# Kernel tuning notes

Measured on AMD Instinct MI355X. Metric: run time of the kernel, lower is better.

## Reference

```python
import jax, jax.numpy as jnp
import numpy as np

N = 50000   # nodes
E = 800000  # edges
D = 200     # h_dim == out_dim
R = 500     # num_rels
L = 2       # num_hidden_layers
RRELU_SLOPE = (1.0 / 8.0 + 1.0 / 3.0) / 2.0  # eval-mode F.rrelu negative slope


def _rrelu(x):
    return jnp.where(x >= 0, x, x * jnp.float32(RRELU_SLOPE))


def setup_inputs() -> dict:
    key = jax.random.key(0)
    ks = jax.random.split(key, 10)
    s = np.float32(1.0 / np.sqrt(D))  # ~xavier scale
    return {
        "init_ent_emb": jax.random.normal(ks[0], (N, D), jnp.float32),
        "rel_emb": jax.random.normal(ks[1], (R, D), jnp.float32),
        "weight_neighbor": jax.random.normal(ks[2], (L, D, D), jnp.float32) * s,
        "loop_weight": jax.random.normal(ks[3], (L, D, D), jnp.float32) * s,
        "evolve_loop_weight": jax.random.normal(ks[4], (L, D, D), jnp.float32) * s,
        "norm": jax.random.uniform(ks[5], (N, 1), jnp.float32),
        "src": jax.random.randint(ks[6], (E,), 0, N, dtype=jnp.int32),
        "dst": jax.random.randint(ks[7], (E,), 0, N, dtype=jnp.int32),
        "etype": jax.random.randint(ks[8], (E,), 0, R, dtype=jnp.int32),
        "node_id": jnp.arange(N, dtype=jnp.int32),
    }


def reference(init_ent_emb, rel_emb, weight_neighbor, loop_weight,
              evolve_loop_weight, norm, src, dst, etype, node_id):
    # g.ndata['h'] = init_ent_emb[node_id]
    h = init_ent_emb[node_id]                                    # [N, D]
    # mask of nodes with in-degree > 0 (fixed across layers)
    indeg = jnp.zeros((N,), jnp.float32).at[dst].add(1.0)
    has_in = (indeg > 0)[:, None]                                # [N, 1]
    for l in range(L):
        # loop message: loop_weight where in-degree>0, evolve_loop_weight otherwise
        loop_msg = jnp.where(has_in,
                             h @ loop_weight[l],
                             h @ evolve_loop_weight[l])          # [N, D]
        # per-edge message: (h_src + rel_emb[etype]) @ W_neighbor
        msg = (h[src] + rel_emb[etype]) @ weight_neighbor[l]     # [E, D]
        # sum-scatter to destination nodes, then per-node norm (apply_func)
        agg = jax.ops.segment_sum(msg, dst, num_segments=N)      # [N, D]
        h = _rrelu(agg * norm + loop_msg)
    return h
```

## Files before the change

### kernel.cpp

```cpp
#include <hip/hip_runtime.h>

#define D 200
#define RRELU_SLOPE 0.22916666666666666f
#define STRIDE 96
#define PAD 8

typedef unsigned short u16;
typedef unsigned int u32;

using bf16x8 = __attribute__((ext_vector_type(8))) short;
using f32x4  = __attribute__((ext_vector_type(4))) float;

__device__ __forceinline__ float rrelu(float x) {
    return x >= 0.0f ? x : x * RRELU_SLOPE;
}
__device__ __forceinline__ float bf2f(u32 u) {
    union { u32 i; float f; } c; c.i = u << 16; return c.f;
}
__device__ __forceinline__ u32 f2bf(float f) {
    union { float f; u32 i; } c; c.f = f;
    return (c.i + 0x7fffu + ((c.i >> 16) & 1u)) >> 16;
}
__device__ __forceinline__ u32 pack2(float x, float y) {
    return f2bf(x) | (f2bf(y) << 16);
}
__device__ __forceinline__ void gll16(const void* g, void* l) {
    __builtin_amdgcn_global_load_lds((const __attribute__((address_space(1))) void*)g,
                                     (__attribute__((address_space(3))) void*)l,
                                     16, 0, 0);
}

__device__ __forceinline__ void accu4(uint4 q, float* acc) {
    acc[0] += bf2f(q.x & 0xffffu); acc[1] += bf2f(q.x >> 16);
    acc[2] += bf2f(q.y & 0xffffu); acc[3] += bf2f(q.y >> 16);
    acc[4] += bf2f(q.z & 0xffffu); acc[5] += bf2f(q.z >> 16);
    acc[6] += bf2f(q.w & 0xffffu); acc[7] += bf2f(q.w >> 16);
}


__global__ void prep_k(const float* __restrict__ rel, const float* __restrict__ Wn,
                       const float* __restrict__ Wl, u16* __restrict__ relb,
                       u16* __restrict__ Bt, u16* __restrict__ hb0d,
                       u16* __restrict__ hb1d, int* __restrict__ noin_cnt) {
    int i = blockIdx.x * blockDim.x + threadIdx.x;
    if (i == 0) *noin_cnt = 0;
    if (i < 200) { hb0d[i] = 0; hb1d[i] = 0; }
    if (i < 100200) relb[i] = (i < 100000) ? (u16)f2bf(rel[i]) : (u16)0;
    if (i < 2 * 256 * 416) {
        int l = i / (256 * 416);
        int rem = i % (256 * 416);
        int c = rem / 416;
        int k = rem % 416;
        float v = 0.0f;
        if (c < 200 && k < 400)
            v = (k < 200) ? Wn[(size_t)l * 40000 + k * 200 + c]
                          : Wl[(size_t)l * 40000 + (k - 200) * 200 + c];
        Bt[i] = (u16)f2bf(v);
    }
}


__global__ void scatter_k(const int* __restrict__ dst, const int* __restrict__ src,
                          const int* __restrict__ etype, int* __restrict__ cnt,
                          u32* __restrict__ ep, int E) {
    int e = blockIdx.x * blockDim.x + threadIdx.x;
    if (e < E) {
        int d = dst[e];
        int c = atomicAdd(&cnt[d], 1);
        if (c < STRIDE)
            ep[(size_t)d * STRIDE + c] = (u32)src[e] | ((u32)etype[e] << 17);
    }
}

__global__ void pad_k(const int* __restrict__ cnt, u32* __restrict__ ep, u32 dummy,
                      int* __restrict__ noin, int* __restrict__ noin_cnt, int N) {
    int v = blockIdx.x * blockDim.x + threadIdx.x;
    if (v >= N) return;
    int c = cnt[v];
    if (c == 0) noin[atomicAdd(noin_cnt, 1)] = v;
    int e = (c + PAD - 1) & ~(PAD - 1);
    for (int i = c; i < e; ++i) ep[(size_t)v * STRIDE + i] = dummy;
}


__global__ void gather_k(const float* __restrict__ init, const int* __restrict__ nid,
                         u16* __restrict__ hb, int N) {
    int lane = threadIdx.x & 63;
    int v = blockIdx.x * 4 + (threadIdx.x >> 6);
    if (v >= N || lane >= 50) return;
    float4 f = *(const float4*)(init + (size_t)nid[v] * D + lane * 4);
    uint2 o;
    o.x = pack2(f.x, f.y);
    o.y = pack2(f.z, f.w);
    *(uint2*)(hb + (size_t)v * D + lane * 4) = o;
}


__global__ void gagg0_k(const u16* __restrict__ hb, const u16* __restrict__ relb,
                        const u32* __restrict__ ep, const int* __restrict__ cnt,
                        const float* __restrict__ norm,
                        u16* __restrict__ aggb, u16* __restrict__ relsumb, int N) {
    int lane = threadIdx.x & 63;
    int wave = threadIdx.x >> 6;
    int li = lane & 31;
    int v = blockIdx.x * 8 + wave * 2 + (lane >> 5);
    if (v >= N || li >= 25) return;
    size_t lo = (size_t)li * 8;
    const u16* hbL = hb + lo;
    const u16* rbL = relb + lo;
    int c = cnt[v];
    int rv = (c + PAD - 1) >> 3;
    int beg = v * STRIDE;
    float a[8] = {}, rr[8] = {};
    for (int r = 0; r < rv; ++r) {
        int ib = beg + r * PAD;
        u32 p[8];
#pragma unroll
        for (int j = 0; j < 8; ++j) p[j] = ep[ib + j];
        uint4 qh[8], qr[8];
#pragma unroll
        for (int j = 0; j < 8; ++j)
            qh[j] = *(const uint4*)(hbL + (size_t)(p[j] & 0x1FFFF) * D);
#pragma unroll
        for (int j = 0; j < 8; ++j)
            qr[j] = *(const uint4*)(rbL + (size_t)((p[j] >> 17) & 0x3FF) * D);
#pragma unroll
        for (int j = 0; j < 8; ++j) { accu4(qh[j], a); accu4(qr[j], rr); }
    }
    uint4 rs;
    rs.x = pack2(rr[0], rr[1]); rs.y = pack2(rr[2], rr[3]);
    rs.z = pack2(rr[4], rr[5]); rs.w = pack2(rr[6], rr[7]);
    *(uint4*)(relsumb + (size_t)v * D + lo) = rs;
    float nv = norm[v];
    uint4 o;
    o.x = pack2((a[0] + rr[0]) * nv, (a[1] + rr[1]) * nv);
    o.y = pack2((a[2] + rr[2]) * nv, (a[3] + rr[3]) * nv);
    o.z = pack2((a[4] + rr[4]) * nv, (a[5] + rr[5]) * nv);
    o.w = pack2((a[6] + rr[6]) * nv, (a[7] + rr[7]) * nv);
    *(uint4*)(aggb + (size_t)v * D + lo) = o;
}


__global__ void gagg1_k(const u16* __restrict__ hb, const u32* __restrict__ ep,
                        const int* __restrict__ cnt, const float* __restrict__ norm,
                        const u16* __restrict__ addb, u16* __restrict__ outb, int N) {
    int lane = threadIdx.x & 63;
    int wave = threadIdx.x >> 6;
    int li = lane & 31;
    int v = blockIdx.x * 8 + wave * 2 + (lane >> 5);
    if (v >= N || li >= 25) return;
    size_t lo = (size_t)li * 8;
    const u16* hbL = hb + lo;
    int c = cnt[v];
    int rv = (c + PAD - 1) >> 3;
    int beg = v * STRIDE;
    float a[8] = {};
    for (int r = 0; r < rv; ++r) {
        int ib = beg + r * PAD;
        u32 p[8];
#pragma unroll
        for (int j = 0; j < 8; ++j) p[j] = ep[ib + j];
        uint4 q[8];
#pragma unroll
        for (int j = 0; j < 8; ++j)
            q[j] = *(const uint4*)(hbL + (size_t)(p[j] & 0x1FFFF) * D);
#pragma unroll
        for (int j = 0; j < 8; ++j) accu4(q[j], a);
    }
    {
        uint4 q = *(const uint4*)(addb + (size_t)v * D + lo);
        accu4(q, a);
    }
    float nv = norm[v];
    uint4 o;
    o.x = pack2(a[0] * nv, a[1] * nv);
    o.y = pack2(a[2] * nv, a[3] * nv);
    o.z = pack2(a[4] * nv, a[5] * nv);
    o.w = pack2(a[6] * nv, a[7] * nv);
    *(uint4*)(outb + (size_t)v * D + lo) = o;
}


__global__ __launch_bounds__(256) void gemm_k(
        const u16* __restrict__ Aagg, const u16* __restrict__ Ah,
        const u16* __restrict__ Bt,
        float* __restrict__ outF, u16* __restrict__ outB, int M) {
    __shared__ __align__(16) u16 As[128 * 32];
    __shared__ __align__(16) u16 Bs[64 * 32];
    int tid = threadIdx.x;
    int lane = tid & 63;
    int wave = tid >> 6;
    int rowBase = blockIdx.x * 128;
    int colBase = blockIdx.y * 64;
    int wr = (wave >> 1) * 64;
    int wc = (wave & 1) * 32;
    int m = lane & 15;
    int kq = (lane >> 4) * 8;

    int srow = tid >> 2;
    int kg = (tid & 3) * 8;

    u16* ldsA0 = As + ((size_t)(wave * 64) * 8);
    u16* ldsA1 = As + ((size_t)(256 + wave * 64) * 8);
    u16* ldsB  = Bs + ((size_t)(wave * 64) * 8);

    f32x4 acc[4][2] = {};

    for (int k0 = 0; k0 < 416; k0 += 32) {
        int k = k0 + kg;
        {
            const u16* g0 = (k < 200) ? Aagg + (size_t)(rowBase + srow) * D + k
                                      : Ah + (size_t)(rowBase + srow) * D + (k - 200);
            gll16(g0, ldsA0);
            const u16* g1 = (k < 200) ? Aagg + (size_t)(rowBase + srow + 64) * D + k
                                      : Ah + (size_t)(rowBase + srow + 64) * D + (k - 200);
            gll16(g1, ldsA1);
            const u16* gb = Bt + (size_t)(colBase + srow) * 416 + k;
            gll16(gb, ldsB);
        }
        __syncthreads();

        bf16x8 a0 = *(const bf16x8*)(As + (wr + m) * 32 + kq);
        bf16x8 a1 = *(const bf16x8*)(As + (wr + 16 + m) * 32 + kq);
        bf16x8 a2 = *(const bf16x8*)(As + (wr + 32 + m) * 32 + kq);
        bf16x8 a3 = *(const bf16x8*)(As + (wr + 48 + m) * 32 + kq);
        bf16x8 b0 = *(const bf16x8*)(Bs + (wc + m) * 32 + kq);
        bf16x8 b1 = *(const bf16x8*)(Bs + (wc + 16 + m) * 32 + kq);
        acc[0][0] = __builtin_amdgcn_mfma_f32_16x16x32_bf16(a0, b0, acc[0][0], 0, 0, 0);
        acc[0][1] = __builtin_amdgcn_mfma_f32_16x16x32_bf16(a0, b1, acc[0][1], 0, 0, 0);
        acc[1][0] = __builtin_amdgcn_mfma_f32_16x16x32_bf16(a1, b0, acc[1][0], 0, 0, 0);
        acc[1][1] = __builtin_amdgcn_mfma_f32_16x16x32_bf16(a1, b1, acc[1][1], 0, 0, 0);
        acc[2][0] = __builtin_amdgcn_mfma_f32_16x16x32_bf16(a2, b0, acc[2][0], 0, 0, 0);
        acc[2][1] = __builtin_amdgcn_mfma_f32_16x16x32_bf16(a2, b1, acc[2][1], 0, 0, 0);
        acc[3][0] = __builtin_amdgcn_mfma_f32_16x16x32_bf16(a3, b0, acc[3][0], 0, 0, 0);
        acc[3][1] = __builtin_amdgcn_mfma_f32_16x16x32_bf16(a3, b1, acc[3][1], 0, 0, 0);
        __syncthreads();
    }

    int cRow = (lane >> 4) * 4;
    int cCol = lane & 15;
#pragma unroll
    for (int i = 0; i < 4; ++i) {
#pragma unroll
        for (int j = 0; j < 2; ++j) {
            int col = colBase + wc + j * 16 + cCol;
            if (col >= 200) continue;
#pragma unroll
            for (int r = 0; r < 4; ++r) {
                int row = rowBase + wr + i * 16 + cRow + r;
                if (row < M) {
                    float val = rrelu(acc[i][j][r]);
                    if (outF) outF[(size_t)row * D + col] = val;
                    if (outB) outB[(size_t)row * D + col] = (u16)f2bf(val);
                }
            }
        }
    }
}


__global__ void fixup_k(const u16* __restrict__ hb, const float* __restrict__ We,
                        const int* __restrict__ noin, const int* __restrict__ noin_cnt,
                        float* __restrict__ outF, u16* __restrict__ outB) {
    int cnt = *noin_cnt;
    for (int i = blockIdx.x; i < cnt; i += gridDim.x) {
        int v = noin[i];
        int j = threadIdx.x;
        if (j < D) {
            float acc = 0.0f;
            for (int k = 0; k < D; ++k)
                acc += bf2f(hb[(size_t)v * D + k]) * We[(size_t)k * D + j];
            float r = rrelu(acc);
            if (outF) outF[(size_t)v * D + j] = r;
            if (outB) outB[(size_t)v * D + j] = (u16)f2bf(r);
        }
    }
}

extern "C" void kernel_launch(void* const* d_in, const int* in_sizes, int n_in,
                              void* d_out, int out_size, void* d_ws, size_t ws_size,
                              hipStream_t stream) {
    const float* init  = (const float*)d_in[0];
    const float* rel   = (const float*)d_in[1];
    const float* Wn    = (const float*)d_in[2];
    const float* Wl    = (const float*)d_in[3];
    const float* We    = (const float*)d_in[4];
    const float* norm  = (const float*)d_in[5];
    const int* src     = (const int*)d_in[6];
    const int* dst     = (const int*)d_in[7];
    const int* etype   = (const int*)d_in[8];
    const int* node_id = (const int*)d_in[9];
    float* out = (float*)d_out;

    int N = in_sizes[5];
    int E = in_sizes[6];
    size_t NP = (size_t)N + 256;

    char* w = (char*)d_ws;
    auto carve = [&](size_t bytes) {
        char* p = w;
        w += (bytes + 255) & ~(size_t)255;
        return p;
    };
    u16* hb0     = (u16*)carve(NP * D * sizeof(u16));
    u16* hb1     = (u16*)carve(NP * D * sizeof(u16));
    u16* aggb    = (u16*)carve(NP * D * sizeof(u16));
    u16* relsumb = (u16*)carve((size_t)N * D * sizeof(u16));
    u16* relb    = (u16*)carve((size_t)501 * D * sizeof(u16));
    u16* Bt      = (u16*)carve((size_t)2 * 256 * 416 * sizeof(u16));
    int* cnt     = (int*)carve((size_t)N * sizeof(int));
    u32* epack   = (u32*)carve((size_t)N * STRIDE * sizeof(u32));
    int* noin    = (int*)carve((size_t)N * sizeof(int));
    int* noin_cnt = (int*)carve(sizeof(int));

    (void)hipMemsetAsync(cnt, 0, (size_t)N * sizeof(int), stream);

    int prepN = 2 * 256 * 416;
    prep_k<<<(prepN + 255) / 256, 256, 0, stream>>>(rel, Wn, Wl, relb, Bt,
                                                    hb0 + (size_t)N * D,
                                                    hb1 + (size_t)N * D, noin_cnt);
    scatter_k<<<(E + 255) / 256, 256, 0, stream>>>(dst, src, etype, cnt, epack, E);
    u32 dummy = (u32)N | (500u << 17);
    pad_k<<<(N + 255) / 256, 256, 0, stream>>>(cnt, epack, dummy, noin, noin_cnt, N);
    gather_k<<<(N + 3) / 4, 256, 0, stream>>>(init, node_id, hb0, N);

    dim3 gg((N + 127) / 128, 4);

    gagg0_k<<<(N + 7) / 8, 256, 0, stream>>>(hb0, relb, epack, cnt, norm,
                                             aggb, relsumb, N);
    gemm_k<<<gg, 256, 0, stream>>>(aggb, hb0, Bt, nullptr, hb1, N);
    fixup_k<<<8, 256, 0, stream>>>(hb0, We, noin, noin_cnt, nullptr, hb1);

    gagg1_k<<<(N + 7) / 8, 256, 0, stream>>>(hb1, epack, cnt, norm,
                                             relsumb, aggb, N);
    gemm_k<<<gg, 256, 0, stream>>>(aggb, hb1, Bt + 256 * 416, out, nullptr, N);
    fixup_k<<<8, 256, 0, stream>>>(hb1, We + D * D, noin, noin_cnt, out, nullptr);
}
```

Baseline: 375.8 us.

## Restructure gather-aggregate kernels as persistent one-node-per-wave loops with packed accumulation

Both edge-aggregation kernels now give one whole wave per node, with 50 lanes each loading 4 bf16 values via 8-byte loads, instead of half-wave per node with 16-byte loads. The grid becomes a fixed 2048-block persistent loop over nodes. The next group of packed edge indices is prefetched while the current gathers are in flight, and accumulation uses float2 vectors so packed adds can be emitted. The edge buffer gets extra padding so the prefetch can read past the end safely. The aim is better memory-level parallelism and less launch and tail imbalance, at the cost of smaller per-lane loads and more waves per node.

```diff
diff --git a/kernel.cpp b/kernel.cpp
--- a/kernel.cpp
+++ b/kernel.cpp
@@ -10,6 +10,7 @@
 
 using bf16x8 = __attribute__((ext_vector_type(8))) short;
 using f32x4  = __attribute__((ext_vector_type(4))) float;
+using f32x2  = __attribute__((ext_vector_type(2))) float;
 
 __device__ __forceinline__ float rrelu(float x) {
     return x >= 0.0f ? x : x * RRELU_SLOPE;
@@ -30,11 +31,12 @@
                                      16, 0, 0);
 }
 
-__device__ __forceinline__ void accu4(uint4 q, float* acc) {
-    acc[0] += bf2f(q.x & 0xffffu); acc[1] += bf2f(q.x >> 16);
-    acc[2] += bf2f(q.y & 0xffffu); acc[3] += bf2f(q.y >> 16);
-    acc[4] += bf2f(q.z & 0xffffu); acc[5] += bf2f(q.z >> 16);
-    acc[6] += bf2f(q.w & 0xffffu); acc[7] += bf2f(q.w >> 16);
+__device__ __forceinline__ void accw(u32 w, f32x2& acc) {
+    union { u32 i; float f; } lo, hi;
+    lo.i = w << 16;
+    hi.i = w & 0xffff0000u;
+    f32x2 t; t[0] = lo.f; t[1] = hi.f;
+    acc += t;
 }
 
 
@@ -96,88 +98,94 @@
 }
 
 
-__global__ void gagg0_k(const u16* __restrict__ hb, const u16* __restrict__ relb,
-                        const u32* __restrict__ ep, const int* __restrict__ cnt,
-                        const float* __restrict__ norm,
-                        u16* __restrict__ aggb, u16* __restrict__ relsumb, int N) {
+__global__ __launch_bounds__(256) void gagg0_k(
+        const u16* __restrict__ hb, const u16* __restrict__ relb,
+        const u32* __restrict__ ep, const int* __restrict__ cnt,
+        const float* __restrict__ norm,
+        u16* __restrict__ aggb, u16* __restrict__ relsumb, int N, int NW) {
     int lane = threadIdx.x & 63;
-    int wave = threadIdx.x >> 6;
-    int li = lane & 31;
-    int v = blockIdx.x * 8 + wave * 2 + (lane >> 5);
-    if (v >= N || li >= 25) return;
-    size_t lo = (size_t)li * 8;
-    const u16* hbL = hb + lo;
-    const u16* rbL = relb + lo;
-    int c = cnt[v];
-    int rv = (c + PAD - 1) >> 3;
-    int beg = v * STRIDE;
-    float a[8] = {}, rr[8] = {};
-    for (int r = 0; r < rv; ++r) {
-        int ib = beg + r * PAD;
+    int wid = __builtin_amdgcn_readfirstlane(blockIdx.x * 4 + (threadIdx.x >> 6));
+    if (lane >= 50) return;
+    const u16* hbL = hb + lane * 4;
+    const u16* rbL = relb + lane * 4;
+    for (int v = wid; v < N; v += NW) {
+        int c = cnt[v];
+        if (c > STRIDE) c = STRIDE;
+        int rv = (c + PAD - 1) >> 3;
+        const u32* pp = ep + (size_t)v * STRIDE;
+        f32x2 a0 = {0.0f, 0.0f}, a1 = {0.0f, 0.0f};
+        f32x2 r0 = {0.0f, 0.0f}, r1 = {0.0f, 0.0f};
         u32 p[8];
 #pragma unroll
-        for (int j = 0; j < 8; ++j) p[j] = ep[ib + j];
-        uint4 qh[8], qr[8];
-#pragma unroll
-        for (int j = 0; j < 8; ++j)
-            qh[j] = *(const uint4*)(hbL + (size_t)(p[j] & 0x1FFFF) * D);
-#pragma unroll
-        for (int j = 0; j < 8; ++j)
-            qr[j] = *(const uint4*)(rbL + (size_t)((p[j] >> 17) & 0x3FF) * D);
-#pragma unroll
-        for (int j = 0; j < 8; ++j) { accu4(qh[j], a); accu4(qr[j], rr); }
-    }
-    uint4 rs;
-    rs.x = pack2(rr[0], rr[1]); rs.y = pack2(rr[2], rr[3]);
-    rs.z = pack2(rr[4], rr[5]); rs.w = pack2(rr[6], rr[7]);
-    *(uint4*)(relsumb + (size_t)v * D + lo) = rs;
-    float nv = norm[v];
-    uint4 o;
-    o.x = pack2((a[0] + rr[0]) * nv, (a[1] + rr[1]) * nv);
-    o.y = pack2((a[2] + rr[2]) * nv, (a[3] + rr[3]) * nv);
-    o.z = pack2((a[4] + rr[4]) * nv, (a[5] + rr[5]) * nv);
-    o.w = pack2((a[6] + rr[6]) * nv, (a[7] + rr[7]) * nv);
-    *(uint4*)(aggb + (size_t)v * D + lo) = o;
-}
-
-
-__global__ void gagg1_k(const u16* __restrict__ hb, const u32* __restrict__ ep,
-                        const int* __restrict__ cnt, const float* __restrict__ norm,
-                        const u16* __restrict__ addb, u16* __restrict__ outb, int N) {
+        for (int j = 0; j < 8; ++j) p[j] = pp[j];
+        for (int r = 0; r < rv; ++r) {
+            uint2 qh[8], qr[8];
+#pragma unroll
+            for (int j = 0; j < 8; ++j)
+                qh[j] = *(const uint2*)(hbL + (size_t)(p[j] & 0x1FFFFu) * D);
+#pragma unroll
+            for (int j = 0; j < 8; ++j)
+                qr[j] = *(const uint2*)(rbL + (size_t)((p[j] >> 17) & 0x3FFu) * D);
+#pragma unroll
+            for (int j = 0; j < 8; ++j) p[j] = pp[(size_t)(r + 1) * 8 + j];
+#pragma unroll
+            for (int j = 0; j < 8; ++j) {
+                accw(qh[j].x, a0); accw(qh[j].y, a1);
+                accw(qr[j].x, r0); accw(qr[j].y, r1);
+            }
+        }
+        uint2 rs;
+        rs.x = pack2(r0[0], r0[1]);
+        rs.y = pack2(r1[0], r1[1]);
+        *(uint2*)(relsumb + (size_t)v * D + lane * 4) = rs;
+        float nv = norm[v];
+        uint2 o;
+        o.x = pack2((a0[0] + r0[0]) * nv, (a0[1] + r0[1]) * nv);
+        o.y = pack2((a1[0] + r1[0]) * nv, (a1[1] + r1[1]) * nv);
+        *(uint2*)(aggb + (size_t)v * D + lane * 4) = o;
+    }
+}
+
+
+__global__ __launch_bounds__(256) void gagg1_k(
+        const u16* __restrict__ hb, const u32* __restrict__ ep,
+        const int* __restrict__ cnt, const float* __restrict__ norm,
+        const u16* __restrict__ addb, u16* __restrict__ outb, int N, int NW) {
     int lane = threadIdx.x & 63;
-    int wave = threadIdx.x >> 6;
-    int li = lane & 31;
-    int v = blockIdx.x * 8 + wave * 2 + (lane >> 5);
-    if (v >= N || li >= 25) return;
-    size_t lo = (size_t)li * 8;
-    const u16* hbL = hb + lo;
-    int c = cnt[v];
-    int rv = (c + PAD - 1) >> 3;
-    int beg = v * STRIDE;
-    float a[8] = {};
-    for (int r = 0; r < rv; ++r) {
-        int ib = beg + r * PAD;
+    int wid = __builtin_amdgcn_readfirstlane(blockIdx.x * 4 + (threadIdx.x >> 6));
+    if (lane >= 50) return;
+    const u16* hbL = hb + lane * 4;
+    for (int v = wid; v < N; v += NW) {
+        int c = cnt[v];
+        if (c > STRIDE) c = STRIDE;
+        int rv = (c + PAD - 1) >> 3;
+        const u32* pp = ep + (size_t)v * STRIDE;
+        f32x2 a0 = {0.0f, 0.0f}, a1 = {0.0f, 0.0f};
         u32 p[8];
 #pragma unroll
-        for (int j = 0; j < 8; ++j) p[j] = ep[ib + j];
-        uint4 q[8];
-#pragma unroll
-        for (int j = 0; j < 8; ++j)
-            q[j] = *(const uint4*)(hbL + (size_t)(p[j] & 0x1FFFF) * D);
-#pragma unroll
-        for (int j = 0; j < 8; ++j) accu4(q[j], a);
-    }
-    {
-        uint4 q = *(const uint4*)(addb + (size_t)v * D + lo);
-        accu4(q, a);
-    }
-    float nv = norm[v];
-    uint4 o;
-    o.x = pack2(a[0] * nv, a[1] * nv);
-    o.y = pack2(a[2] * nv, a[3] * nv);
-    o.z = pack2(a[4] * nv, a[5] * nv);
-    o.w = pack2(a[6] * nv, a[7] * nv);
-    *(uint4*)(outb + (size_t)v * D + lo) = o;
+        for (int j = 0; j < 8; ++j) p[j] = pp[j];
+        for (int r = 0; r < rv; ++r) {
+            uint2 q[8];
+#pragma unroll
+            for (int j = 0; j < 8; ++j)
+                q[j] = *(const uint2*)(hbL + (size_t)(p[j] & 0x1FFFFu) * D);
+#pragma unroll
+            for (int j = 0; j < 8; ++j) p[j] = pp[(size_t)(r + 1) * 8 + j];
+#pragma unroll
+            for (int j = 0; j < 8; ++j) {
+                accw(q[j].x, a0); accw(q[j].y, a1);
+            }
+        }
+        {
+            uint2 q = *(const uint2*)(addb + (size_t)v * D + lane * 4);
+            accw(q.x, a0); accw(q.y, a1);
+        }
+        float nv = norm[v];
+        uint2 o;
+        o.x = pack2(a0[0] * nv, a0[1] * nv);
+        o.y = pack2(a1[0] * nv, a1[1] * nv);
+        *(uint2*)(outb + (size_t)v * D + lane * 4) = o;
+    }
 }
 
 
@@ -309,7 +317,7 @@
     u16* relb    = (u16*)carve((size_t)501 * D * sizeof(u16));
     u16* Bt      = (u16*)carve((size_t)2 * 256 * 416 * sizeof(u16));
     int* cnt     = (int*)carve((size_t)N * sizeof(int));
-    u32* epack   = (u32*)carve((size_t)N * STRIDE * sizeof(u32));
+    u32* epack   = (u32*)carve(((size_t)N * STRIDE + PAD) * sizeof(u32));
     int* noin    = (int*)carve((size_t)N * sizeof(int));
     int* noin_cnt = (int*)carve(sizeof(int));
 
@@ -326,13 +334,16 @@
 
     dim3 gg((N + 127) / 128, 4);
 
-    gagg0_k<<<(N + 7) / 8, 256, 0, stream>>>(hb0, relb, epack, cnt, norm,
-                                             aggb, relsumb, N);
+    int gaggBlocks = 2048;
+    int NW = gaggBlocks * 4;
+
+    gagg0_k<<<gaggBlocks, 256, 0, stream>>>(hb0, relb, epack, cnt, norm,
+                                            aggb, relsumb, N, NW);
     gemm_k<<<gg, 256, 0, stream>>>(aggb, hb0, Bt, nullptr, hb1, N);
     fixup_k<<<8, 256, 0, stream>>>(hb0, We, noin, noin_cnt, nullptr, hb1);
 
-    gagg1_k<<<(N + 7) / 8, 256, 0, stream>>>(hb1, epack, cnt, norm,
-                                             relsumb, aggb, N);
+    gagg1_k<<<gaggBlocks, 256, 0, stream>>>(hb1, epack, cnt, norm,
+                                            relsumb, aggb, N, NW);
     gemm_k<<<gg, 256, 0, stream>>>(aggb, hb1, Bt + 256 * 416, out, nullptr, N);
     fixup_k<<<8, 256, 0, stream>>>(hb1, We + D * D, noin, noin_cnt, out, nullptr);
 }
```

After: 381.2 us. No clear change (+1.4%).
